# Performance work log

Hardware: AMD Instinct MI355X
Metric: run time of the kernel (lower is better)

The kernel has to match this reference:

```python
import jax, jax.numpy as jnp
import numpy as np

TEMPERATURE = 0.7
REDUCTION = "mean"
MARGIN = 0.5  # the '+0.5' shift inside exp in the original


def setup_inputs() -> dict:
    key = jax.random.key(0)
    k1, k2 = jax.random.split(key)
    projection = jax.random.normal(k1, (8192, 256), dtype=jnp.float32)
    y = jax.random.randint(k2, (8192,), 0, 10, dtype=jnp.int64)
    return {"projection": projection, "y": y}


def reference(projection, y):
    # L2-normalize rows, cosine similarity matrix [n, n]
    n = projection.shape[0]
    proj = projection / jnp.linalg.norm(projection, axis=1, keepdims=True)
    sim = proj @ proj.T

    eq = (y[:, None] == y[None, :]).astype(sim.dtype)
    same = eq - jnp.eye(n, dtype=sim.dtype)   # same class, excluding self
    diff = 1.0 - eq                            # different class

    # Original per-row loop computes log(1 + sum_{j in diff, k in same}
    #   exp((sim[i,j] - sim[i,k] + 0.5)/t)) which separates as
    #   exp(0.5/t) * (sum_j exp(sim[i,j]/t)) * (sum_k exp(-sim[i,k]/t)).
    # Empty set -> the loop substitutes [0], i.e. that factor becomes exp(0)=1.
    A = jnp.sum(diff * jnp.exp(sim / TEMPERATURE), axis=1)
    B = jnp.sum(same * jnp.exp(-sim / TEMPERATURE), axis=1)
    A = jnp.where(jnp.sum(diff, axis=1) > 0, A, 1.0)
    B = jnp.where(jnp.sum(same, axis=1) > 0, B, 1.0)

    loss_per_row = jnp.log1p(jnp.exp(MARGIN / TEMPERATURE) * A * B)
    if REDUCTION == "mean":
        return jnp.mean(loss_per_row)
    return jnp.sum(loss_per_row)
```

## Files before the change

### kernel.cpp

```cpp
#include <hip/hip_runtime.h>
#include <hip/hip_bf16.h>


#define NF 256
#define TINV (1.0f / 0.7f)
#define SC2 2.0609929398439434f

typedef __attribute__((ext_vector_type(8))) short short8;
typedef __attribute__((ext_vector_type(4))) float float4v;

typedef const __attribute__((address_space(1))) unsigned int glb_u32;
typedef __attribute__((address_space(3))) unsigned int lds_u32;

__global__ __launch_bounds__(256)
void k_prep(const float* __restrict__ P, unsigned short* __restrict__ Pn,
            float* __restrict__ AB) {
    int wave = threadIdx.x >> 6, lane = threadIdx.x & 63;
    int row = blockIdx.x * 4 + wave;
    if (threadIdx.x < 8) AB[blockIdx.x * 8 + threadIdx.x] = 0.f;
    float4 v = *(const float4*)(P + (size_t)row * NF + lane * 4);
    float sq = v.x * v.x + v.y * v.y + v.z * v.z + v.w * v.w;
#pragma unroll
    for (int off = 32; off; off >>= 1) sq += __shfl_xor(sq, off, 64);
    float r = rsqrtf(sq);
    __hip_bfloat16 h0 = __float2bfloat16(v.x * r), h1 = __float2bfloat16(v.y * r),
                   h2 = __float2bfloat16(v.z * r), h3 = __float2bfloat16(v.w * r);
    ushort4 o = { *(unsigned short*)&h0, *(unsigned short*)&h1,
                  *(unsigned short*)&h2, *(unsigned short*)&h3 };
    *(ushort4*)(Pn + (size_t)row * NF + lane * 4) = o;
}

__global__ __launch_bounds__(256, 3)
void k_main(const unsigned short* __restrict__ Pn, const int* __restrict__ y,
            float* __restrict__ Aacc, float* __restrict__ Bacc) {
    __shared__ __align__(16) unsigned short Bs[64 * NF];
    __shared__ int yc[512];

    const int tid = threadIdx.x;
    const int I = blockIdx.x >> 4;
    const int G = blockIdx.x & 15;
    const int rb = I * 128, cb0 = G * 512;
    const int lane = tid & 63, wave = tid >> 6;
    const int quad = lane >> 4, l15 = lane & 15;

    yc[tid] = y[cb0 + tid];
    yc[256 + tid] = y[cb0 + 256 + tid];

    const unsigned short* pa = Pn + (size_t)(rb + wave * 32 + l15) * NF + quad * 8;
    short8 afr[2][8];
#pragma unroll
    for (int tr = 0; tr < 2; ++tr)
#pragma unroll
        for (int ks = 0; ks < 8; ++ks)
            afr[tr][ks] = *(const short8*)(pa + (size_t)tr * 16 * NF + ks * 32);

    unsigned yis[2];
#pragma unroll
    for (int tr = 0; tr < 2; ++tr) {
        int4 v = *(const int4*)(y + rb + wave * 32 + tr * 16 + quad * 4);
        yis[tr] = (unsigned)(v.x & 255) | ((unsigned)(v.y & 255) << 8) |
                  ((unsigned)(v.z & 255) << 16) | ((unsigned)(v.w & 255) << 24);
    }

    float rA[2][4], rB[2][4];
#pragma unroll
    for (int tr = 0; tr < 2; ++tr)
#pragma unroll
        for (int r = 0; r < 4; ++r) { rA[tr][r] = 0.f; rB[tr][r] = 0.f; }

#define DMA_CHUNK(c)                                                          \
    {                                                                         \
        _Pragma("unroll")                                                     \
        for (int i = 0; i < 8; ++i) {                                         \
            const int kc = wave * 8 + i;                                      \
            const unsigned short* src =                                       \
                Pn + (size_t)(cb0 + (c) * 64 + lane) * NF + kc * 8;           \
            __builtin_amdgcn_global_load_lds((glb_u32*)src,                   \
                (lds_u32*)&Bs[kc * 512], 16, 0, 0);                           \
        }                                                                     \
    }

    DMA_CHUNK(0)

#pragma unroll 1
    for (int c = 0; c < 8; ++c) {
        __syncthreads();

        float4v acc[2][4];
#pragma unroll
        for (int a = 0; a < 2; ++a)
#pragma unroll
            for (int b = 0; b < 4; ++b) acc[a][b] = (float4v){0.f, 0.f, 0.f, 0.f};

#pragma unroll
        for (int ks = 0; ks < 8; ++ks) {
            short8 fb[4];
#pragma unroll
            for (int tc = 0; tc < 4; ++tc)
                fb[tc] = *(const short8*)&Bs[(ks * 4 + quad) * 512 + (tc * 16 + l15) * 8];
#pragma unroll
            for (int tr = 0; tr < 2; ++tr)
#pragma unroll
                for (int tc = 0; tc < 4; ++tc)
                    acc[tr][tc] = __builtin_amdgcn_mfma_f32_16x16x32_bf16(
                        afr[tr][ks], fb[tc], acc[tr][tc], 0, 0, 0);
        }
        __syncthreads();
        if (c < 7) DMA_CHUNK(c + 1)

#pragma unroll
        for (int tc = 0; tc < 4; ++tc) {
            const int jl = c * 64 + tc * 16 + l15;
            const int yj = yc[jl];
            const int gj = cb0 + jl;
#pragma unroll
            for (int tr = 0; tr < 2; ++tr) {
                const int gi0 = rb + wave * 32 + tr * 16 + quad * 4;
#pragma unroll
                for (int r = 0; r < 4; ++r) {
                    const float s = acc[tr][tc][r];
                    const int cls = (yis[tr] >> (8 * r)) & 255;
                    const bool same = (cls == yj);
                    const float e = exp2f(s * (same ? -SC2 : SC2));
                    rA[tr][r] += same ? 0.f : e;
                    rB[tr][r] += (same && (gi0 + r != gj)) ? e : 0.f;
                }
            }
        }
    }

#pragma unroll
    for (int tr = 0; tr < 2; ++tr)
#pragma unroll
        for (int r = 0; r < 4; ++r) {
#pragma unroll
            for (int off = 1; off < 16; off <<= 1) {
                rA[tr][r] += __shfl_xor(rA[tr][r], off, 64);
                rB[tr][r] += __shfl_xor(rB[tr][r], off, 64);
            }
        }
    if (l15 == 0) {
#pragma unroll
        for (int tr = 0; tr < 2; ++tr)
#pragma unroll
            for (int r = 0; r < 4; ++r) {
                const int gi = rb + wave * 32 + tr * 16 + quad * 4 + r;
                atomicAdd(&Aacc[gi], rA[tr][r]);
                atomicAdd(&Bacc[gi], rB[tr][r]);
            }
    }
}

__global__ __launch_bounds__(1024)
void k_final(const float* __restrict__ Aacc, const float* __restrict__ Bacc,
             const int* __restrict__ y, float* __restrict__ out, int n) {
    __shared__ int hist[16];
    __shared__ float red[16];
    const int tid = threadIdx.x;
    if (tid < 16) hist[tid] = 0;
    __syncthreads();
    int loc[10];
#pragma unroll
    for (int cc = 0; cc < 10; ++cc) loc[cc] = 0;
    for (int i = tid; i < n; i += 1024) {
        const int yv = y[i];
#pragma unroll
        for (int cc = 0; cc < 10; ++cc) {
            unsigned long long m = __ballot(yv == cc);
            if ((tid & 63) == 0) loc[cc] += __popcll(m);
        }
    }
    if ((tid & 63) == 0)
#pragma unroll
        for (int cc = 0; cc < 10; ++cc) atomicAdd(&hist[cc], loc[cc]);
    __syncthreads();
    const float M = __expf(0.5f * TINV);
    float s = 0.f;
    for (int i = tid; i < n; i += 1024) {
        const int cc = hist[y[i] & 15];
        const float a = (n - cc) > 0 ? Aacc[i] : 1.0f;
        const float b = (cc - 1) > 0 ? Bacc[i] : 1.0f;
        s += log1pf(M * a * b);
    }
#pragma unroll
    for (int off = 32; off; off >>= 1) s += __shfl_xor(s, off, 64);
    if ((tid & 63) == 0) red[tid >> 6] = s;
    __syncthreads();
    if (tid == 0) {
        float t = 0.f;
#pragma unroll
        for (int w = 0; w < 16; ++w) t += red[w];
        out[0] = t / (float)n;
    }
}

extern "C" void kernel_launch(void* const* d_in, const int* in_sizes, int n_in,
                              void* d_out, int out_size, void* d_ws, size_t ws_size,
                              hipStream_t stream) {
    const float* P = (const float*)d_in[0];
    const int* y   = (const int*)d_in[1];
    float* out     = (float*)d_out;
    const int n = in_sizes[1];

    unsigned short* Pn = (unsigned short*)d_ws;
    float* Aacc = (float*)((char*)d_ws + (size_t)n * NF * 2);
    float* Bacc = Aacc + n;

    k_prep<<<n / 4, 256, 0, stream>>>(P, Pn, Aacc);
    k_main<<<(n / 128) * (n / 512), 256, 0, stream>>>(Pn, y, Aacc, Bacc);
    k_final<<<1, 1024, 0, stream>>>(Aacc, Bacc, y, out, n);
}
```

Baseline: 135.9 us.

## Exploit symmetry of similarity matrix to compute only upper-triangular tiles

Uses the symmetry of the cosine-similarity matrix to launch only blocks in the upper triangle (row-block 128 x column-block 256). Each tile's exp values are also reduced per column and added to the column rows' A/B accumulators through shared-memory and then global atomics. This roughly halves the MFMA and exp work. The cost is extra per-column shuffles, LDS atomics and global atomics, plus a triangular block-index decode using sqrt. Diagonal tiles skip column accumulation, and the self-exclusion for column sums relies on off-diagonal tiles only.

```diff
diff --git a/kernel.cpp b/kernel.cpp
--- a/kernel.cpp
+++ b/kernel.cpp
@@ -34,39 +34,20 @@
 void k_main(const unsigned short* __restrict__ Pn, const int* __restrict__ y,
             float* __restrict__ Aacc, float* __restrict__ Bacc) {
     __shared__ __align__(16) unsigned short Bs[64 * NF];
-    __shared__ int yc[512];
+    __shared__ int yc[256];
+    __shared__ float colA[256], colB[256];
 
     const int tid = threadIdx.x;
-    const int I = blockIdx.x >> 4;
-    const int G = blockIdx.x & 15;
-    const int rb = I * 128, cb0 = G * 512;
+    int bid = blockIdx.x;
+    int C = (int)((sqrtf(4.0f * (float)bid + 1.0f) - 1.0f) * 0.5f);
+    while (C * (C + 1) > bid) --C;
+    while ((C + 1) * (C + 2) <= bid) ++C;
+    const int I = bid - C * (C + 1);
+    const int rb = I * 128, cb0 = C * 256;
+    const bool colacc = (C > (I >> 1));
+
     const int lane = tid & 63, wave = tid >> 6;
     const int quad = lane >> 4, l15 = lane & 15;
-
-    yc[tid] = y[cb0 + tid];
-    yc[256 + tid] = y[cb0 + 256 + tid];
-
-    const unsigned short* pa = Pn + (size_t)(rb + wave * 32 + l15) * NF + quad * 8;
-    short8 afr[2][8];
-#pragma unroll
-    for (int tr = 0; tr < 2; ++tr)
-#pragma unroll
-        for (int ks = 0; ks < 8; ++ks)
-            afr[tr][ks] = *(const short8*)(pa + (size_t)tr * 16 * NF + ks * 32);
-
-    unsigned yis[2];
-#pragma unroll
-    for (int tr = 0; tr < 2; ++tr) {
-        int4 v = *(const int4*)(y + rb + wave * 32 + tr * 16 + quad * 4);
-        yis[tr] = (unsigned)(v.x & 255) | ((unsigned)(v.y & 255) << 8) |
-                  ((unsigned)(v.z & 255) << 16) | ((unsigned)(v.w & 255) << 24);
-    }
-
-    float rA[2][4], rB[2][4];
-#pragma unroll
-    for (int tr = 0; tr < 2; ++tr)
-#pragma unroll
-        for (int r = 0; r < 4; ++r) { rA[tr][r] = 0.f; rB[tr][r] = 0.f; }
 
 #define DMA_CHUNK(c)                                                          \
     {                                                                         \
@@ -82,8 +63,34 @@
 
     DMA_CHUNK(0)
 
+    yc[tid] = y[cb0 + tid];
+    colA[tid] = 0.f;
+    colB[tid] = 0.f;
+
+    const unsigned short* pa = Pn + (size_t)(rb + wave * 32 + l15) * NF + quad * 8;
+    short8 afr[2][8];
+#pragma unroll
+    for (int tr = 0; tr < 2; ++tr)
+#pragma unroll
+        for (int ks = 0; ks < 8; ++ks)
+            afr[tr][ks] = *(const short8*)(pa + (size_t)tr * 16 * NF + ks * 32);
+
+    unsigned yis[2];
+#pragma unroll
+    for (int tr = 0; tr < 2; ++tr) {
+        int4 v = *(const int4*)(y + rb + wave * 32 + tr * 16 + quad * 4);
+        yis[tr] = (unsigned)(v.x & 255) | ((unsigned)(v.y & 255) << 8) |
+                  ((unsigned)(v.z & 255) << 16) | ((unsigned)(v.w & 255) << 24);
+    }
+
+    float rA[2][4], rB[2][4];
+#pragma unroll
+    for (int tr = 0; tr < 2; ++tr)
+#pragma unroll
+        for (int r = 0; r < 4; ++r) { rA[tr][r] = 0.f; rB[tr][r] = 0.f; }
+
 #pragma unroll 1
-    for (int c = 0; c < 8; ++c) {
+    for (int c = 0; c < 4; ++c) {
         __syncthreads();
 
         float4v acc[2][4];
@@ -106,13 +113,14 @@
                         afr[tr][ks], fb[tc], acc[tr][tc], 0, 0, 0);
         }
         __syncthreads();
-        if (c < 7) DMA_CHUNK(c + 1)
+        if (c < 3) DMA_CHUNK(c + 1)
 
 #pragma unroll
         for (int tc = 0; tc < 4; ++tc) {
             const int jl = c * 64 + tc * 16 + l15;
             const int yj = yc[jl];
             const int gj = cb0 + jl;
+            float ca = 0.f, cbv = 0.f;
 #pragma unroll
             for (int tr = 0; tr < 2; ++tr) {
                 const int gi0 = rb + wave * 32 + tr * 16 + quad * 4;
@@ -124,6 +132,16 @@
                     const float e = exp2f(s * (same ? -SC2 : SC2));
                     rA[tr][r] += same ? 0.f : e;
                     rB[tr][r] += (same && (gi0 + r != gj)) ? e : 0.f;
+                    ca  += same ? 0.f : e;
+                    cbv += same ? e : 0.f;
+                }
+            }
+            if (colacc) {
+                ca  += __shfl_xor(ca, 16, 64);  ca  += __shfl_xor(ca, 32, 64);
+                cbv += __shfl_xor(cbv, 16, 64); cbv += __shfl_xor(cbv, 32, 64);
+                if (quad == 0) {
+                    atomicAdd(&colA[jl], ca);
+                    atomicAdd(&colB[jl], cbv);
                 }
             }
         }
@@ -148,6 +166,12 @@
                 atomicAdd(&Aacc[gi], rA[tr][r]);
                 atomicAdd(&Bacc[gi], rB[tr][r]);
             }
+    }
+
+    if (colacc) {
+        __syncthreads();
+        atomicAdd(&Aacc[cb0 + tid], colA[tid]);
+        atomicAdd(&Bacc[cb0 + tid], colB[tid]);
     }
 }
 
@@ -206,7 +230,8 @@
     float* Aacc = (float*)((char*)d_ws + (size_t)n * NF * 2);
     float* Bacc = Aacc + n;
 
+    const int ng = n / 256;
     k_prep<<<n / 4, 256, 0, stream>>>(P, Pn, Aacc);
-    k_main<<<(n / 128) * (n / 512), 256, 0, stream>>>(Pn, y, Aacc, Bacc);
+    k_main<<<ng * (ng + 1), 256, 0, stream>>>(Pn, y, Aacc, Bacc);
     k_final<<<1, 1024, 0, stream>>>(Aacc, Bacc, y, out, n);
 }
```

After: 146.8 us. 8.1% more time.
